# Performance work log

Measured on AMD Instinct MI355X. Metric: run time of the kernel, lower is better.

## Reference

```python
import jax, jax.numpy as jnp
import numpy as np

NUM_CLASSES = 80
ALPHA = 0.25
GAMMA = 2.0
CONF_T = 0.5
IOU_T = 0.5
N_ANCHORS = 6144


def _pairwise_iou(b):
    # b: [n,4] (x1,y1,x2,y2) -> [n,n] IoU matrix
    area = (b[:, 2] - b[:, 0]) * (b[:, 3] - b[:, 1])
    lt = jnp.maximum(b[:, None, :2], b[None, :, :2])
    rb = jnp.minimum(b[:, None, 2:], b[None, :, 2:])
    wh = jnp.clip(rb - lt, 0.0)
    inter = wh[..., 0] * wh[..., 1]
    return inter / (area[:, None] + area[None, :] - inter)


def _nms(boxes, scores, thr):
    # torchvision-style NMS: returns kept indices in decreasing-score order
    order = jnp.argsort(-scores)
    iou = _pairwise_iou(boxes[order])
    n = boxes.shape[0]
    ar = jnp.arange(n)
    def body(i, supp):
        return supp | ((iou[i] > thr) & (ar > i) & jnp.logical_not(supp[i]))
    supp = jax.lax.fori_loop(0, n, body, jnp.zeros(n, dtype=bool))
    kept_pos = jnp.where(~supp)[0]  # eager: concrete shapes
    return order[kept_pos]


def _make_boxes(tb, floc):
    # tb: [1,1,4] target box; floc: [Nf,2] filtered predicted locations
    # replicates loc_determined with T=1: (tx1*px, ty1*py, tx2*px, ty2*py)
    px, py = floc[:, 0], floc[:, 1]
    return jnp.stack([tb[0, 0, 0] * px, tb[0, 0, 1] * py,
                      tb[0, 0, 2] * px, tb[0, 0, 3] * py], axis=1)


def _smooth_l1_sum(pred, tgt):
    d = jnp.abs(pred - tgt)  # broadcasts [k,C,4] vs [1,1,4]
    return jnp.where(d < 1.0, 0.5 * d * d, d - 0.5).sum()


def setup_inputs() -> dict:
    key = jax.random.key(0)
    k1, k2, k3 = jax.random.split(key, 3)
    locations = jax.random.uniform(k1, (1, N_ANCHORS, 2), dtype=jnp.float32)
    confidences = jax.random.uniform(k2, (1, N_ANCHORS, NUM_CLASSES), dtype=jnp.float32)
    # valid target box (x1<x2, y1<y2) in [0,1]
    target_boxes = jnp.array([[[0.15, 0.2, 0.85, 0.9]]], dtype=jnp.float32)
    target_labels = jax.random.randint(k3, (1,), 0, NUM_CLASSES)
    return {"locations": locations, "confidences": confidences,
            "target_boxes": target_boxes, "target_labels": target_labels}


def reference(locations, confidences, target_boxes, target_labels):
    conf = confidences[0]                       # [N,C]
    scores_max = conf.max(axis=1)
    idx_f = jnp.where(scores_max > CONF_T)[0]   # eager boolean filter
    if idx_f.shape[0] == 0:
        return jnp.float32(0.001)
    floc = locations[0, idx_f, :]               # [Nf,2]
    fconf = conf[idx_f]                         # [Nf,C]
    boxes = _make_boxes(target_boxes, floc)     # [Nf,4] (pred_loc_final)
    score = fconf[:, 0]                         # class-0 score, as in original
    keep = _nms(boxes, score, IOU_T)            # kept indices
    if keep.shape[0] == 0:
        return jnp.float32(0.001)
    matched_loc = boxes[keep]                   # [M,4]
    matched_conf = fconf[keep]                  # [M,C]
    k = target_labels.shape[0]                  # = 1
    topv, topi = jax.lax.top_k(matched_conf.T, k)  # per-class top-k over dim 0
    topv, topi = topv.T, topi.T                 # [k,C]
    pred_bin = (topv[:, 0] > 0.5).astype(jnp.float32)  # [k]
    mloc = matched_loc[topi]                    # [k,C,4]
    loc_loss = _smooth_l1_sum(mloc, target_boxes)
    # F.cross_entropy with 1-D float input/target = probabilities mode, unbatched
    ce = -(target_labels.astype(jnp.float32) * jax.nn.log_softmax(pred_bin)).sum()
    focal = ALPHA * (1.0 - jnp.exp(-ce)) ** GAMMA * ce
    # original bug preserved: num_positives = sum of kept *indices*
    num_pos = keep.sum().astype(jnp.float32)
    return (loc_loss + focal) / num_pos
```

## Files before the change

### kernel.cpp

```cpp
#include <hip/hip_runtime.h>
#include <stdint.h>

#define N_ANCHORS 6144
#define NUM_CLASSES 80
#define NWORDS 96
#define NTILES 24

__device__ unsigned long long g_mask[(size_t)N_ANCHORS * NWORDS];
__device__ float4 g_sbox[N_ANCHORS];
__device__ int    g_rpart[NTILES][N_ANCHORS];
__device__ int    g_fpart[NTILES][N_ANCHORS];
__device__ int    g_sAnchor[N_ANCHORS];
__device__ int    g_sFi[N_ANCHORS];
__device__ int    g_keptPos[N_ANCHORS];
__device__ int    g_F, g_K, g_np, g_done;
__device__ float  g_loss;

__device__ __forceinline__ unsigned long long shfl64(unsigned long long v, int l) {
    return __shfl(v, l, 64);
}

__device__ __forceinline__ float anchor_key(const float* __restrict__ conf, int i, bool& valid) {
    const float4* cp4 = (const float4*)(conf + (size_t)i * NUM_CLASSES);
    float4 v0 = cp4[0];
    float score = v0.x;
    float m = fmaxf(fmaxf(v0.x, v0.y), fmaxf(v0.z, v0.w));
    #pragma unroll
    for (int c = 1; c < NUM_CLASSES / 4; ++c) {
        float4 v = cp4[c];
        m = fmaxf(m, fmaxf(fmaxf(v.x, v.y), fmaxf(v.z, v.w)));
    }
    valid = m > 0.5f;
    return valid ? score : -1.0f;
}

__global__ void __launch_bounds__(256) k_rank(const float* __restrict__ conf) {
    __shared__ float skey[256];
    int y = blockIdx.y;
    int j0 = y * 256;
    bool vj;
    skey[threadIdx.x] = anchor_key(conf, j0 + threadIdx.x, vj);
    int i = blockIdx.x * 256 + threadIdx.x;
    bool vi;
    float ki = anchor_key(conf, i, vi);
    __syncthreads();
    int r = 0, f = 0;
    #pragma unroll 8
    for (int jj = 0; jj < 256; ++jj) {
        float kj = skey[jj];
        int j = j0 + jj;
        bool valid_j = kj >= 0.0f;
        r += (kj > ki) || (kj == ki && j < i && valid_j);
        f += (j < i) && valid_j;
    }
    g_rpart[y][i] = r;
    g_fpart[y][i] = f;
}

__global__ void __launch_bounds__(256) k_scatter(const float* __restrict__ loc,
                                                 const float* __restrict__ conf,
                                                 const float* __restrict__ tb) {
    int i = blockIdx.x * 256 + threadIdx.x;
    bool vi;
    float ki = anchor_key(conf, i, vi);
    (void)ki;
    int r = 0, f = 0;
    #pragma unroll
    for (int y = 0; y < NTILES; ++y) { r += g_rpart[y][i]; f += g_fpart[y][i]; }
    if (vi) {
        float px = loc[2 * i], py = loc[2 * i + 1];
        float4 b;
        b.x = __fmul_rn(tb[0], px);
        b.y = __fmul_rn(tb[1], py);
        b.z = __fmul_rn(tb[2], px);
        b.w = __fmul_rn(tb[3], py);
        g_sbox[r] = b;
        g_sAnchor[r] = i;
        g_sFi[r] = f;
    }
    if (i == N_ANCHORS - 1) g_F = f + (vi ? 1 : 0);
}

__global__ void __launch_bounds__(256) k_mask(void) {
    int wave = (blockIdx.x * 256 + threadIdx.x) >> 6;
    int lane = threadIdx.x & 63;
    if (wave >= N_ANCHORS) return;
    int i = wave;
    float4 bi = g_sbox[i];
    float areai = __fmul_rn(bi.z - bi.x, bi.w - bi.y);
    unsigned long long* row = g_mask + (size_t)i * NWORDS;
    for (int w = (i >> 6); w < NWORDS; ++w) {
        float4 bj = g_sbox[w * 64 + lane];
        float areaj = __fmul_rn(bj.z - bj.x, bj.w - bj.y);
        float lx = fmaxf(bi.x, bj.x), ly = fmaxf(bi.y, bj.y);
        float rx = fminf(bi.z, bj.z), ry = fminf(bi.w, bj.w);
        float iw = fmaxf(rx - lx, 0.0f), ih = fmaxf(ry - ly, 0.0f);
        float inter = __fmul_rn(iw, ih);
        float denom = __fsub_rn(__fadd_rn(areai, areaj), inter);
        float iou = __fdiv_rn(inter, denom);
        unsigned long long bits = __ballot(iou > 0.5f);
        if (lane == 0) row[w] = bits;
    }
}

#define SCAN_B 32
__global__ void __launch_bounds__(64, 1) k_scan(void) {
    int lane = threadIdx.x;
    int F = g_F;
    if (lane == 0) { g_loss = 0.0f; g_np = 0; g_done = 0; }
    auto initw = [&](int w) -> unsigned long long {
        long long lo = (long long)w * 64, hi = lo + 64;
        if (F <= lo) return ~0ull;
        if (F >= hi) return 0ull;
        return (~0ull) << (F - lo);
    };
    unsigned long long remv0 = initw(lane);
    unsigned long long remv1 = (lane < 32) ? initw(64 + lane) : ~0ull;
    unsigned long long kept0 = 0, kept1 = 0;
    int lastPos = -1;

    __shared__ int slots[SCAN_B];

    while (true) {
        unsigned long long c0 = ~remv0;
        unsigned long long c1 = (lane < 32) ? ~remv1 : 0ull;
        {
            long long lo = (long long)lane << 6;
            if (lastPos >= lo + 63)      c0 = 0ull;
            else if (lastPos >= lo)      c0 &= (~0ull) << (int)(lastPos - lo + 1);
        }
        if (lane < 32) {
            long long lo = (long long)(64 + lane) << 6;
            if (lastPos >= lo + 63)      c1 = 0ull;
            else if (lastPos >= lo)      c1 &= (~0ull) << (int)(lastPos - lo + 1);
        }
        int n0 = __popcll(c0), n1 = __popcll(c1);
        int x0 = n0, x1 = n1;
        for (int ofs = 1; ofs < 64; ofs <<= 1) {
            int y0 = __shfl_up(x0, ofs, 64);
            int y1 = __shfl_up(x1, ofs, 64);
            if (lane >= ofs) { x0 += y0; x1 += y1; }
        }
        int tot0 = __shfl(x0, 63, 64);
        int tot1 = __shfl(x1, 63, 64);
        int total = tot0 + tot1;
        if (total == 0) break;
        int off0 = x0 - n0;
        int off1 = tot0 + (x1 - n1);
        {
            unsigned long long wd = c0; int r = off0;
            while (wd && r < SCAN_B) { int b = __builtin_ctzll(wd); slots[r++] = lane * 64 + b; wd &= wd - 1; }
        }
        if (lane < 32) {
            unsigned long long wd = c1; int r = off1;
            while (wd && r < SCAN_B) { int b = __builtin_ctzll(wd); slots[r++] = (64 + lane) * 64 + b; wd &= wd - 1; }
        }
        __syncthreads();
        int nb = (total < SCAN_B) ? total : SCAN_B;
        int pos[SCAN_B];
        #pragma unroll
        for (int q = 0; q < SCAN_B; ++q) pos[q] = (q < nb) ? slots[q] : -1;
        __syncthreads();

        unsigned long long r0[SCAN_B], r1[SCAN_B];
        #pragma unroll
        for (int q = 0; q < SCAN_B; ++q) {
            if (pos[q] >= 0) {
                const unsigned long long* rp = g_mask + (size_t)pos[q] * NWORDS;
                r0[q] = rp[lane];
                r1[q] = (lane < 32) ? rp[64 + lane] : 0ull;
            } else { r0[q] = 0ull; r1[q] = 0ull; }
        }

        #pragma unroll
        for (int q = 0; q < SCAN_B; ++q) {
            if (pos[q] >= 0) {
                int w = pos[q] >> 6, b = pos[q] & 63;
                unsigned long long cw = (w < 64) ? shfl64(remv0, w) : shfl64(remv1, w - 64);
                if (!((cw >> b) & 1ull)) {
                    remv0 |= r0[q];
                    if (lane < 32) remv1 |= r1[q];
                    if (w < 64) { if (lane == w) kept0 |= 1ull << b; }
                    else        { if (lane == w - 64) kept1 |= 1ull << b; }
                }
                lastPos = pos[q];
            }
        }
    }

    int c0 = __popcll(kept0);
    int c1 = (lane < 32) ? __popcll(kept1) : 0;
    int x0 = c0, x1 = c1;
    for (int ofs = 1; ofs < 64; ofs <<= 1) {
        int y0 = __shfl_up(x0, ofs, 64);
        int y1 = __shfl_up(x1, ofs, 64);
        if (lane >= ofs) { x0 += y0; x1 += y1; }
    }
    int t0 = __shfl(x0, 63, 64);
    int t1 = __shfl(x1, 63, 64);
    int off = x0 - c0;
    unsigned long long wd = kept0;
    while (wd) { int b = __builtin_ctzll(wd); g_keptPos[off++] = lane * 64 + b; wd &= wd - 1; }
    off = t0 + (x1 - c1);
    wd = kept1;
    while (wd) { int b = __builtin_ctzll(wd); g_keptPos[off++] = (64 + lane) * 64 + b; wd &= wd - 1; }
    if (lane == 0) g_K = t0 + t1;
}

__global__ void __launch_bounds__(64) k_loss(const float* __restrict__ conf, const float* __restrict__ tb,
                                             float* __restrict__ out) {
    int c = blockIdx.x;
    int lane = threadIdx.x;
    int K = g_K;
    float bv = -3.402823466e+38f;
    int bk = 0x7fffffff;
    int np = 0;
    for (int k = lane; k < K; k += 64) {
        int p = g_keptPos[k];
        int a = g_sAnchor[p];
        float v = conf[(size_t)a * NUM_CLASSES + c];
        if (v > bv || (v == bv && k < bk)) { bv = v; bk = k; }
        if (c == 0) np += g_sFi[p];
    }
    for (int ofs = 32; ofs > 0; ofs >>= 1) {
        float ov = __shfl_down(bv, ofs, 64);
        int ok = __shfl_down(bk, ofs, 64);
        if (ov > bv || (ov == bv && ok < bk)) { bv = ov; bk = ok; }
    }
    if (c == 0) {
        for (int ofs = 32; ofs > 0; ofs >>= 1) np += __shfl_down(np, ofs, 64);
        if (lane == 0) atomicExch(&g_np, np);
    }
    if (lane == 0) {
        if (K > 0) {
            float4 b = g_sbox[g_keptPos[bk]];
            float t0 = tb[0], t1 = tb[1], t2 = tb[2], t3 = tb[3];
            float l = 0.0f, d;
            d = fabsf(b.x - t0); l += (d < 1.0f) ? 0.5f * d * d : d - 0.5f;
            d = fabsf(b.y - t1); l += (d < 1.0f) ? 0.5f * d * d : d - 0.5f;
            d = fabsf(b.z - t2); l += (d < 1.0f) ? 0.5f * d * d : d - 0.5f;
            d = fabsf(b.w - t3); l += (d < 1.0f) ? 0.5f * d * d : d - 0.5f;
            atomicAdd(&g_loss, l);
        }
        __threadfence();
        int done = atomicAdd(&g_done, 1);
        if (done == NUM_CLASSES - 1) {
            float total = atomicAdd(&g_loss, 0.0f);
            int npv = atomicAdd(&g_np, 0);
            out[0] = (g_F == 0 || K == 0) ? 0.001f : total / (float)npv;
        }
    }
}

extern "C" void kernel_launch(void* const* d_in, const int* in_sizes, int n_in,
                              void* d_out, int out_size, void* d_ws, size_t ws_size,
                              hipStream_t stream) {
    const float* loc  = (const float*)d_in[0];
    const float* conf = (const float*)d_in[1];
    const float* tb   = (const float*)d_in[2];
    float* out = (float*)d_out;

    k_rank<<<dim3(NTILES, NTILES), 256, 0, stream>>>(conf);
    k_scatter<<<NTILES, 256, 0, stream>>>(loc, conf, tb);
    k_mask<<<(N_ANCHORS * 64) / 256, 256, 0, stream>>>();
    k_scan<<<1, 64, 0, stream>>>();
    k_loss<<<NUM_CLASSES, 64, 0, stream>>>(conf, tb, out);
}
```

Measured before the change: 164.8 us.

## Stage NMS mask rows via LDS with intra-batch conflict resolution, fuse loss into scan

The serial NMS scan now loads each batch of up to 32 candidate mask rows directly into LDS with global_load_lds. It then resolves keep decisions inside the batch through a per-lane conflict bitmask and a short shuffle loop, replacing the per-candidate shuffle of remv words. The separate 80-block loss kernel is folded into the single-wave scan kernel. That kernel computes the per-class argmax over kept anchors, the smooth-L1 sum and num_pos directly, which removes one launch plus its global atomics and completion counter. The cost is that the loss work now runs on one wave instead of 80 blocks, and the code relies on hand-placed waitcnt asm for correctness.

```diff
diff --git a/kernel.cpp b/kernel.cpp
--- a/kernel.cpp
+++ b/kernel.cpp
@@ -5,16 +5,16 @@
 #define NUM_CLASSES 80
 #define NWORDS 96
 #define NTILES 24
-
-__device__ unsigned long long g_mask[(size_t)N_ANCHORS * NWORDS];
+#define SCAN_B 32
+#define ROWSTRIDE 128
+
+__device__ unsigned long long g_mask[(size_t)N_ANCHORS * NWORDS + 64];
 __device__ float4 g_sbox[N_ANCHORS];
 __device__ int    g_rpart[NTILES][N_ANCHORS];
 __device__ int    g_fpart[NTILES][N_ANCHORS];
 __device__ int    g_sAnchor[N_ANCHORS];
 __device__ int    g_sFi[N_ANCHORS];
-__device__ int    g_keptPos[N_ANCHORS];
-__device__ int    g_F, g_K, g_np, g_done;
-__device__ float  g_loss;
+__device__ int    g_F;
 
 __device__ __forceinline__ unsigned long long shfl64(unsigned long long v, int l) {
     return __shfl(v, l, 64);
@@ -103,11 +103,15 @@
     }
 }
 
-#define SCAN_B 32
-__global__ void __launch_bounds__(64, 1) k_scan(void) {
+__global__ void __launch_bounds__(64, 1) k_scan(const float* __restrict__ conf,
+                                                const float* __restrict__ tb,
+                                                float* __restrict__ out) {
+    __shared__ alignas(16) unsigned long long rowbuf[SCAN_B][ROWSTRIDE];
+    __shared__ int slots[SCAN_B];
+    __shared__ int keptLds[N_ANCHORS];
     int lane = threadIdx.x;
     int F = g_F;
-    if (lane == 0) { g_loss = 0.0f; g_np = 0; g_done = 0; }
+    if (lane < SCAN_B) slots[lane] = 0;
     auto initw = [&](int w) -> unsigned long long {
         long long lo = (long long)w * 64, hi = lo + 64;
         if (F <= lo) return ~0ull;
@@ -119,8 +123,6 @@
     unsigned long long kept0 = 0, kept1 = 0;
     int lastPos = -1;
 
-    __shared__ int slots[SCAN_B];
-
     while (true) {
         unsigned long long c0 = ~remv0;
         unsigned long long c1 = (lane < 32) ? ~remv1 : 0ull;
@@ -145,6 +147,7 @@
         int tot1 = __shfl(x1, 63, 64);
         int total = tot0 + tot1;
         if (total == 0) break;
+        int nb = (total < SCAN_B) ? total : SCAN_B;
         int off0 = x0 - n0;
         int off1 = tot0 + (x1 - n1);
         {
@@ -155,37 +158,50 @@
             unsigned long long wd = c1; int r = off1;
             while (wd && r < SCAN_B) { int b = __builtin_ctzll(wd); slots[r++] = (64 + lane) * 64 + b; wd &= wd - 1; }
         }
-        __syncthreads();
-        int nb = (total < SCAN_B) ? total : SCAN_B;
-        int pos[SCAN_B];
-        #pragma unroll
-        for (int q = 0; q < SCAN_B; ++q) pos[q] = (q < nb) ? slots[q] : -1;
-        __syncthreads();
-
-        unsigned long long r0[SCAN_B], r1[SCAN_B];
-        #pragma unroll
-        for (int q = 0; q < SCAN_B; ++q) {
-            if (pos[q] >= 0) {
-                const unsigned long long* rp = g_mask + (size_t)pos[q] * NWORDS;
-                r0[q] = rp[lane];
-                r1[q] = (lane < 32) ? rp[64 + lane] : 0ull;
-            } else { r0[q] = 0ull; r1[q] = 0ull; }
-        }
-
-        #pragma unroll
-        for (int q = 0; q < SCAN_B; ++q) {
-            if (pos[q] >= 0) {
-                int w = pos[q] >> 6, b = pos[q] & 63;
-                unsigned long long cw = (w < 64) ? shfl64(remv0, w) : shfl64(remv1, w - 64);
-                if (!((cw >> b) & 1ull)) {
-                    remv0 |= r0[q];
-                    if (lane < 32) remv1 |= r1[q];
+        asm volatile("s_waitcnt lgkmcnt(0)" ::: "memory");
+        int myPos = slots[(lane < SCAN_B) ? lane : 0];
+        int myW = myPos >> 6, myB = myPos & 63;
+
+        for (int p = 0; p < nb; ++p) {
+            int P = __shfl(myPos, p, 64);
+            const unsigned long long* rp = g_mask + (size_t)P * NWORDS;
+            __builtin_amdgcn_global_load_lds((const uint32_t*)rp + lane * 4,
+                                             (uint32_t*)&rowbuf[p][0], 16, 0, 0);
+        }
+        asm volatile("s_waitcnt vmcnt(0)" ::: "memory");
+
+        uint32_t conflict = 0;
+        for (int p0 = 0; p0 < nb; p0 += 8) {
+            unsigned long long w[8];
+            #pragma unroll
+            for (int q = 0; q < 8; ++q) w[q] = rowbuf[p0 + q][myW];
+            #pragma unroll
+            for (int q = 0; q < 8; ++q)
+                if (p0 + q < nb) conflict |= (uint32_t)((w[q] >> myB) & 1ull) << (p0 + q);
+        }
+        conflict &= (lane < nb) ? ((1u << lane) - 1u) : 0u;
+
+        uint32_t keptm = 0;
+        for (int p = 0; p < nb; ++p) {
+            uint32_t cp = (uint32_t)__shfl((int)conflict, p, 64);
+            if ((cp & keptm) == 0) keptm |= 1u << p;
+        }
+
+        for (int p0 = 0; p0 < nb; p0 += 8) {
+            #pragma unroll
+            for (int q = 0; q < 8; ++q) {
+                int p = p0 + q;
+                if (p < nb && ((keptm >> p) & 1u)) {
+                    remv0 |= rowbuf[p][lane];
+                    if (lane < 32) remv1 |= rowbuf[p][64 + lane];
+                    int P = __shfl(myPos, p, 64);
+                    int w = P >> 6, b = P & 63;
                     if (w < 64) { if (lane == w) kept0 |= 1ull << b; }
                     else        { if (lane == w - 64) kept1 |= 1ull << b; }
                 }
-                lastPos = pos[q];
             }
         }
+        lastPos = __shfl(myPos, nb - 1, 64);
     }
 
     int c0 = __popcll(kept0);
@@ -200,56 +216,72 @@
     int t1 = __shfl(x1, 63, 64);
     int off = x0 - c0;
     unsigned long long wd = kept0;
-    while (wd) { int b = __builtin_ctzll(wd); g_keptPos[off++] = lane * 64 + b; wd &= wd - 1; }
+    while (wd) { int b = __builtin_ctzll(wd); keptLds[off++] = lane * 64 + b; wd &= wd - 1; }
     off = t0 + (x1 - c1);
     wd = kept1;
-    while (wd) { int b = __builtin_ctzll(wd); g_keptPos[off++] = (64 + lane) * 64 + b; wd &= wd - 1; }
-    if (lane == 0) g_K = t0 + t1;
-}
-
-__global__ void __launch_bounds__(64) k_loss(const float* __restrict__ conf, const float* __restrict__ tb,
-                                             float* __restrict__ out) {
-    int c = blockIdx.x;
-    int lane = threadIdx.x;
-    int K = g_K;
-    float bv = -3.402823466e+38f;
-    int bk = 0x7fffffff;
-    int np = 0;
+    while (wd) { int b = __builtin_ctzll(wd); keptLds[off++] = (64 + lane) * 64 + b; wd &= wd - 1; }
+    int K = t0 + t1;
+
+    if (F == 0 || K == 0) { if (lane == 0) out[0] = 0.001f; return; }
+    asm volatile("s_waitcnt lgkmcnt(0)" ::: "memory");
+
+    int* aLds = (int*)&rowbuf[0][0];
+    int npPart = 0;
     for (int k = lane; k < K; k += 64) {
-        int p = g_keptPos[k];
-        int a = g_sAnchor[p];
-        float v = conf[(size_t)a * NUM_CLASSES + c];
-        if (v > bv || (v == bv && k < bk)) { bv = v; bk = k; }
-        if (c == 0) np += g_sFi[p];
-    }
-    for (int ofs = 32; ofs > 0; ofs >>= 1) {
-        float ov = __shfl_down(bv, ofs, 64);
-        int ok = __shfl_down(bk, ofs, 64);
-        if (ov > bv || (ov == bv && ok < bk)) { bv = ov; bk = ok; }
-    }
-    if (c == 0) {
-        for (int ofs = 32; ofs > 0; ofs >>= 1) np += __shfl_down(np, ofs, 64);
-        if (lane == 0) atomicExch(&g_np, np);
-    }
+        int p = keptLds[k];
+        aLds[k] = g_sAnchor[p];
+        npPart += g_sFi[p];
+    }
+    asm volatile("s_waitcnt lgkmcnt(0) vmcnt(0)" ::: "memory");
+    int Kpad = (K + 7) & ~7;
     if (lane == 0) {
-        if (K > 0) {
-            float4 b = g_sbox[g_keptPos[bk]];
-            float t0 = tb[0], t1 = tb[1], t2 = tb[2], t3 = tb[3];
-            float l = 0.0f, d;
-            d = fabsf(b.x - t0); l += (d < 1.0f) ? 0.5f * d * d : d - 0.5f;
-            d = fabsf(b.y - t1); l += (d < 1.0f) ? 0.5f * d * d : d - 0.5f;
-            d = fabsf(b.z - t2); l += (d < 1.0f) ? 0.5f * d * d : d - 0.5f;
-            d = fabsf(b.w - t3); l += (d < 1.0f) ? 0.5f * d * d : d - 0.5f;
-            atomicAdd(&g_loss, l);
-        }
-        __threadfence();
-        int done = atomicAdd(&g_done, 1);
-        if (done == NUM_CLASSES - 1) {
-            float total = atomicAdd(&g_loss, 0.0f);
-            int npv = atomicAdd(&g_np, 0);
-            out[0] = (g_F == 0 || K == 0) ? 0.001f : total / (float)npv;
-        }
-    }
+        int alast = aLds[K - 1];
+        for (int k = K; k < Kpad; ++k) aLds[k] = alast;
+    }
+    asm volatile("s_waitcnt lgkmcnt(0)" ::: "memory");
+    for (int ofs = 32; ofs > 0; ofs >>= 1) npPart += __shfl_down(npPart, ofs, 64);
+    int np = __shfl(npPart, 0, 64);
+
+    float bv0 = -3.402823466e+38f, bv1 = -3.402823466e+38f;
+    int bk0 = 0, bk1 = 0;
+    for (int k0 = 0; k0 < Kpad; k0 += 8) {
+        int av[8]; float va[8], vb[8];
+        #pragma unroll
+        for (int q = 0; q < 8; ++q) av[q] = aLds[k0 + q];
+        #pragma unroll
+        for (int q = 0; q < 8; ++q) va[q] = conf[(size_t)av[q] * NUM_CLASSES + lane];
+        if (lane < 16) {
+            #pragma unroll
+            for (int q = 0; q < 8; ++q) vb[q] = conf[(size_t)av[q] * NUM_CLASSES + 64 + lane];
+        }
+        #pragma unroll
+        for (int q = 0; q < 8; ++q)
+            if (va[q] > bv0) { bv0 = va[q]; bk0 = k0 + q; }
+        if (lane < 16) {
+            #pragma unroll
+            for (int q = 0; q < 8; ++q)
+                if (vb[q] > bv1) { bv1 = vb[q]; bk1 = k0 + q; }
+        }
+    }
+
+    float tv0 = tb[0], tv1 = tb[1], tv2 = tb[2], tv3 = tb[3];
+    float s, d;
+    {
+        float4 bb = g_sbox[keptLds[bk0]];
+        d = fabsf(bb.x - tv0); s  = (d < 1.0f) ? 0.5f * d * d : d - 0.5f;
+        d = fabsf(bb.y - tv1); s += (d < 1.0f) ? 0.5f * d * d : d - 0.5f;
+        d = fabsf(bb.z - tv2); s += (d < 1.0f) ? 0.5f * d * d : d - 0.5f;
+        d = fabsf(bb.w - tv3); s += (d < 1.0f) ? 0.5f * d * d : d - 0.5f;
+    }
+    if (lane < 16) {
+        float4 bb = g_sbox[keptLds[bk1]];
+        d = fabsf(bb.x - tv0); s += (d < 1.0f) ? 0.5f * d * d : d - 0.5f;
+        d = fabsf(bb.y - tv1); s += (d < 1.0f) ? 0.5f * d * d : d - 0.5f;
+        d = fabsf(bb.z - tv2); s += (d < 1.0f) ? 0.5f * d * d : d - 0.5f;
+        d = fabsf(bb.w - tv3); s += (d < 1.0f) ? 0.5f * d * d : d - 0.5f;
+    }
+    for (int ofs = 32; ofs > 0; ofs >>= 1) s += __shfl_down(s, ofs, 64);
+    if (lane == 0) out[0] = s / (float)np;
 }
 
 extern "C" void kernel_launch(void* const* d_in, const int* in_sizes, int n_in,
@@ -263,6 +295,5 @@
     k_rank<<<dim3(NTILES, NTILES), 256, 0, stream>>>(conf);
     k_scatter<<<NTILES, 256, 0, stream>>>(loc, conf, tb);
     k_mask<<<(N_ANCHORS * 64) / 256, 256, 0, stream>>>();
-    k_scan<<<1, 64, 0, stream>>>();
-    k_loss<<<NUM_CLASSES, 64, 0, stream>>>(conf, tb, out);
-}
+    k_scan<<<1, 64, 0, stream>>>(conf, tb, out);
+}
```

Result: slower. 181.1 us (+9.9%).

## Stage NMS candidate mask rows in LDS and resolve intra-batch conflicts via bitmasks

Applied to the files above, without the earlier changes.

The serial NMS scan kernel now copies each batch of up to 32 candidate mask rows directly into shared memory with global_load_lds, in place of holding them in registers. It then builds a per-candidate conflict bitmask and settles which candidates are kept with a scalar readlane loop. Only the kept rows are ORed into the removal vector, eight at a time. The prefix scans are also packed into a single 32-bit shuffle and readlane, which cuts shuffle count on this single-wave critical path, at the cost of LDS traffic and more intricate control flow.

```diff
diff --git a/kernel.cpp b/kernel.cpp
--- a/kernel.cpp
+++ b/kernel.cpp
@@ -5,8 +5,10 @@
 #define NUM_CLASSES 80
 #define NWORDS 96
 #define NTILES 24
-
-__device__ unsigned long long g_mask[(size_t)N_ANCHORS * NWORDS];
+#define SCAN_B 32
+#define ROWSTRIDE 128
+
+__device__ unsigned long long g_mask[(size_t)N_ANCHORS * NWORDS + 64];
 __device__ float4 g_sbox[N_ANCHORS];
 __device__ int    g_rpart[NTILES][N_ANCHORS];
 __device__ int    g_fpart[NTILES][N_ANCHORS];
@@ -15,10 +17,6 @@
 __device__ int    g_keptPos[N_ANCHORS];
 __device__ int    g_F, g_K, g_np, g_done;
 __device__ float  g_loss;
-
-__device__ __forceinline__ unsigned long long shfl64(unsigned long long v, int l) {
-    return __shfl(v, l, 64);
-}
 
 __device__ __forceinline__ float anchor_key(const float* __restrict__ conf, int i, bool& valid) {
     const float4* cp4 = (const float4*)(conf + (size_t)i * NUM_CLASSES);
@@ -103,11 +101,13 @@
     }
 }
 
-#define SCAN_B 32
 __global__ void __launch_bounds__(64, 1) k_scan(void) {
+    __shared__ alignas(16) unsigned long long rowbuf[SCAN_B][ROWSTRIDE];
+    __shared__ int slots[SCAN_B];
     int lane = threadIdx.x;
     int F = g_F;
     if (lane == 0) { g_loss = 0.0f; g_np = 0; g_done = 0; }
+    if (lane < SCAN_B) slots[lane] = 0;
     auto initw = [&](int w) -> unsigned long long {
         long long lo = (long long)w * 64, hi = lo + 64;
         if (F <= lo) return ~0ull;
@@ -119,8 +119,6 @@
     unsigned long long kept0 = 0, kept1 = 0;
     int lastPos = -1;
 
-    __shared__ int slots[SCAN_B];
-
     while (true) {
         unsigned long long c0 = ~remv0;
         unsigned long long c1 = (lane < 32) ? ~remv1 : 0ull;
@@ -135,18 +133,18 @@
             else if (lastPos >= lo)      c1 &= (~0ull) << (int)(lastPos - lo + 1);
         }
         int n0 = __popcll(c0), n1 = __popcll(c1);
-        int x0 = n0, x1 = n1;
+        int xp = (n0 << 16) | n1;
         for (int ofs = 1; ofs < 64; ofs <<= 1) {
-            int y0 = __shfl_up(x0, ofs, 64);
-            int y1 = __shfl_up(x1, ofs, 64);
-            if (lane >= ofs) { x0 += y0; x1 += y1; }
-        }
-        int tot0 = __shfl(x0, 63, 64);
-        int tot1 = __shfl(x1, 63, 64);
+            int y = __shfl_up(xp, ofs, 64);
+            if (lane >= ofs) xp += y;
+        }
+        int lastxp = __builtin_amdgcn_readlane(xp, 63);
+        int tot0 = lastxp >> 16, tot1 = lastxp & 0xffff;
         int total = tot0 + tot1;
         if (total == 0) break;
-        int off0 = x0 - n0;
-        int off1 = tot0 + (x1 - n1);
+        int nb = (total < SCAN_B) ? total : SCAN_B;
+        int off0 = (xp >> 16) - n0;
+        int off1 = tot0 + ((xp & 0xffff) - n1);
         {
             unsigned long long wd = c0; int r = off0;
             while (wd && r < SCAN_B) { int b = __builtin_ctzll(wd); slots[r++] = lane * 64 + b; wd &= wd - 1; }
@@ -156,52 +154,78 @@
             while (wd && r < SCAN_B) { int b = __builtin_ctzll(wd); slots[r++] = (64 + lane) * 64 + b; wd &= wd - 1; }
         }
         __syncthreads();
-        int nb = (total < SCAN_B) ? total : SCAN_B;
-        int pos[SCAN_B];
-        #pragma unroll
-        for (int q = 0; q < SCAN_B; ++q) pos[q] = (q < nb) ? slots[q] : -1;
-        __syncthreads();
-
-        unsigned long long r0[SCAN_B], r1[SCAN_B];
-        #pragma unroll
-        for (int q = 0; q < SCAN_B; ++q) {
-            if (pos[q] >= 0) {
-                const unsigned long long* rp = g_mask + (size_t)pos[q] * NWORDS;
-                r0[q] = rp[lane];
-                r1[q] = (lane < 32) ? rp[64 + lane] : 0ull;
-            } else { r0[q] = 0ull; r1[q] = 0ull; }
-        }
-
-        #pragma unroll
-        for (int q = 0; q < SCAN_B; ++q) {
-            if (pos[q] >= 0) {
-                int w = pos[q] >> 6, b = pos[q] & 63;
-                unsigned long long cw = (w < 64) ? shfl64(remv0, w) : shfl64(remv1, w - 64);
-                if (!((cw >> b) & 1ull)) {
-                    remv0 |= r0[q];
-                    if (lane < 32) remv1 |= r1[q];
+        int myPos = slots[(lane < SCAN_B) ? lane : 0];
+        int myW = myPos >> 6, myB = myPos & 63;
+
+        for (int p = 0; p < nb; ++p) {
+            int P = __builtin_amdgcn_readlane(myPos, p);
+            const unsigned long long* rp = g_mask + (size_t)P * NWORDS;
+            __builtin_amdgcn_global_load_lds((const uint32_t*)rp + lane * 4,
+                                             (uint32_t*)&rowbuf[p][0], 16, 0, 0);
+        }
+        asm volatile("s_waitcnt vmcnt(0)" ::: "memory");
+        __builtin_amdgcn_sched_barrier(0);
+
+        uint32_t conflict = 0;
+        for (int p0 = 0; p0 < nb; p0 += 8) {
+            unsigned long long w[8];
+            #pragma unroll
+            for (int q = 0; q < 8; ++q) w[q] = rowbuf[p0 + q][myW];
+            #pragma unroll
+            for (int q = 0; q < 8; ++q)
+                if (p0 + q < nb) conflict |= (uint32_t)((w[q] >> myB) & 1ull) << (p0 + q);
+        }
+        conflict &= (lane < nb) ? ((1u << lane) - 1u) : 0u;
+
+        uint32_t keptm = 0;
+        for (int p = 0; p < nb; ++p) {
+            uint32_t cp = (uint32_t)__builtin_amdgcn_readlane((int)conflict, p);
+            if ((cp & keptm) == 0) keptm |= 1u << p;
+        }
+
+        uint32_t km = keptm;
+        while (km) {
+            int kidx[8]; bool kv[8];
+            #pragma unroll
+            for (int q = 0; q < 8; ++q) {
+                kv[q] = (km != 0);
+                kidx[q] = kv[q] ? __builtin_ctz(km) : 0;
+                if (km) km &= km - 1;
+            }
+            unsigned long long a0[8], a1[8];
+            #pragma unroll
+            for (int q = 0; q < 8; ++q) {
+                a0[q] = kv[q] ? rowbuf[kidx[q]][lane] : 0ull;
+                a1[q] = (kv[q] && lane < 32) ? rowbuf[kidx[q]][64 + lane] : 0ull;
+            }
+            #pragma unroll
+            for (int q = 0; q < 8; ++q) { remv0 |= a0[q]; if (lane < 32) remv1 |= a1[q]; }
+            #pragma unroll
+            for (int q = 0; q < 8; ++q) {
+                if (kv[q]) {
+                    int P = __builtin_amdgcn_readlane(myPos, kidx[q]);
+                    int w = P >> 6, b = P & 63;
                     if (w < 64) { if (lane == w) kept0 |= 1ull << b; }
                     else        { if (lane == w - 64) kept1 |= 1ull << b; }
                 }
-                lastPos = pos[q];
             }
         }
+        lastPos = __builtin_amdgcn_readlane(myPos, nb - 1);
     }
 
     int c0 = __popcll(kept0);
     int c1 = (lane < 32) ? __popcll(kept1) : 0;
-    int x0 = c0, x1 = c1;
+    int xp = (c0 << 16) | c1;
     for (int ofs = 1; ofs < 64; ofs <<= 1) {
-        int y0 = __shfl_up(x0, ofs, 64);
-        int y1 = __shfl_up(x1, ofs, 64);
-        if (lane >= ofs) { x0 += y0; x1 += y1; }
-    }
-    int t0 = __shfl(x0, 63, 64);
-    int t1 = __shfl(x1, 63, 64);
-    int off = x0 - c0;
+        int y = __shfl_up(xp, ofs, 64);
+        if (lane >= ofs) xp += y;
+    }
+    int lastxp = __builtin_amdgcn_readlane(xp, 63);
+    int t0 = lastxp >> 16, t1 = lastxp & 0xffff;
+    int off = (xp >> 16) - c0;
     unsigned long long wd = kept0;
     while (wd) { int b = __builtin_ctzll(wd); g_keptPos[off++] = lane * 64 + b; wd &= wd - 1; }
-    off = t0 + (x1 - c1);
+    off = t0 + ((xp & 0xffff) - c1);
     wd = kept1;
     while (wd) { int b = __builtin_ctzll(wd); g_keptPos[off++] = (64 + lane) * 64 + b; wd &= wd - 1; }
     if (lane == 0) g_K = t0 + t1;
```

Measured after the change: 167.7 us. About the same (+1.7%).
